# Optimization experiments

Measured on AMD Instinct MI355X. Metric: run time of the kernel, lower is better.

The kernel has to match this reference:

```python
import jax, jax.numpy as jnp
import numpy as np


def color_bin(x, n_bins):
    """Per-image 3D color histogram over n_bins**3 flat bins.
    x: [B, 3, H, W] float in ~[-1, 1]. Returns [B, n_bins**3] float32.
    """
    B, C, H, W = x.shape
    n_tot = n_bins ** 3
    # torch color_bins: i*(2/n_bins) - 1 for i in 1..n_bins-1
    boundaries = jnp.arange(1, n_bins, dtype=jnp.float32) * (2.0 / n_bins) - 1.0
    # torch.bucketize(right=False) == searchsorted side='left'
    idx = jnp.searchsorted(boundaries, x.reshape(B, C, H * W), side='left')  # [B,3,HW] int
    scale = jnp.array([1, n_bins, n_bins ** 2], dtype=idx.dtype)
    flat = jnp.einsum('bcp,c->bp', idx, scale)  # [B, HW], values in [0, n_tot)
    # torch.histc(bins, n_tot, min=0, max=n_tot-1) on exact integers == bincount
    hist = jax.vmap(lambda f: jnp.bincount(f, length=n_tot))(flat)
    return hist.astype(jnp.float32) / (H * W)


def setup_inputs() -> dict:
    key = jax.random.key(0)
    k1, k2 = jax.random.split(key)
    inp = jax.random.normal(k1, (8, 3, 1024, 1024), dtype=jnp.float32)
    style = jax.random.normal(k2, (1, 3, 1024, 1024), dtype=jnp.float32)
    return {"input": inp, "style_image": style, "n_bins": 16}


def reference(input, style_image, n_bins):
    # target histogram from the style image (detached in torch; ints anyway)
    target = color_bin(style_image, n_bins).squeeze(0)  # [n_tot]
    cols = color_bin(input, n_bins)                     # [B, n_tot]
    # F.l1_loss(cols, target.repeat(B, 1)) with mean reduction
    loss = jnp.mean(jnp.abs(cols - target[None, :]))
    return loss
```

## Files before the change

### kernel.cpp

```cpp
#include <hip/hip_runtime.h>

#define HW      (1024 * 1024)
#define HW4     (HW / 4)
#define NBINS   4096
#define NIMG    9
#define BPI     128
#define THREADS 256
#define F4_PER_BLOCK (HW4 / BPI)
#define NSTAGE  (F4_PER_BLOCK / (2 * THREADS))
#define RBLOCKS 256

typedef float f4 __attribute__((ext_vector_type(4)));

__device__ __forceinline__ int bin16(float x) {
    int lo = 0;
    if (0.0f < x) lo = 8;
    if ((float)(lo + 4) * 0.125f - 1.0f < x) lo += 4;
    if ((float)(lo + 2) * 0.125f - 1.0f < x) lo += 2;
    if ((float)(lo + 1) * 0.125f - 1.0f < x) lo += 1;
    return lo;
}

__device__ __forceinline__ int bin3(float r, float g, float b) {
    return bin16(r) + 16 * bin16(g) + 256 * bin16(b);
}

__device__ __forceinline__ void acc4(int* lh, f4 r, f4 g, f4 b) {
    atomicAdd(&lh[bin3(r.x, g.x, b.x)], 1);
    atomicAdd(&lh[bin3(r.y, g.y, b.y)], 1);
    atomicAdd(&lh[bin3(r.z, g.z, b.z)], 1);
    atomicAdd(&lh[bin3(r.w, g.w, b.w)], 1);
}

__global__ __launch_bounds__(THREADS, 4) void hist_kernel(
        const float* __restrict__ input,
        const float* __restrict__ style,
        unsigned short* __restrict__ part,
        unsigned long long* __restrict__ gsum) {
    __shared__ int lh[NBINS];
    const int img = blockIdx.y;
    const int blk = blockIdx.x;
    if (img == 8 && blk == 0 && threadIdx.x == 0) *gsum = 0ULL;
    const float* base = (img < 8) ? (input + (size_t)img * 3 * HW) : style;

    for (int i = threadIdx.x; i < NBINS; i += THREADS) lh[i] = 0;
    __syncthreads();

    const f4* c0 = (const f4*)(base);
    const f4* c1 = (const f4*)(base + HW);
    const f4* c2 = (const f4*)(base + 2 * HW);
    const int start = blk * F4_PER_BLOCK + threadIdx.x;

    f4 buf[2][6];
    auto load_stage = [&](int s, f4* d) {
        const int p0 = start + s * 2 * THREADS;
        const int p1 = p0 + THREADS;
        d[0] = c0[p0]; d[1] = c1[p0]; d[2] = c2[p0];
        d[3] = c0[p1]; d[4] = c1[p1]; d[5] = c2[p1];
    };

    load_stage(0, buf[0]);
#pragma unroll
    for (int s = 0; s < NSTAGE; ++s) {
        if (s + 1 < NSTAGE) load_stage(s + 1, buf[(s + 1) & 1]);
        f4* d = buf[s & 1];
        acc4(lh, d[0], d[1], d[2]);
        acc4(lh, d[3], d[4], d[5]);
    }
    __syncthreads();

    uint4* dst = (uint4*)(part + ((size_t)img * BPI + blk) * NBINS);
    for (int i = threadIdx.x; i < NBINS / 8; i += THREADS) {
        uint4 v;
        v.x = (unsigned)lh[8 * i]     | ((unsigned)lh[8 * i + 1] << 16);
        v.y = (unsigned)lh[8 * i + 2] | ((unsigned)lh[8 * i + 3] << 16);
        v.z = (unsigned)lh[8 * i + 4] | ((unsigned)lh[8 * i + 5] << 16);
        v.w = (unsigned)lh[8 * i + 6] | ((unsigned)lh[8 * i + 7] << 16);
        dst[i] = v;
    }
}

__global__ __launch_bounds__(THREADS) void reduce_loss_kernel(
        const unsigned short* __restrict__ part,
        unsigned long long* __restrict__ gsum,
        float* __restrict__ out) {
    __shared__ int tred[4][16];
    __shared__ int tgt[16];
    __shared__ int warr[4];
    const int lane = threadIdx.x & 63;
    const int w    = threadIdx.x >> 6;
    const int c    = lane & 1;
    const int p    = lane >> 1;
    const int b0   = blockIdx.x * 16;

    auto qptr = [&](int img, int pg) {
        return (const uint4*)(part + ((size_t)(img * BPI + pg) * NBINS)
                              + b0 + 8 * c);
    };

    {
        uint4 v = *qptr(8, p + 32 * w);
        int v8[8];
        v8[0] = v.x & 0xFFFF; v8[1] = v.x >> 16;
        v8[2] = v.y & 0xFFFF; v8[3] = v.y >> 16;
        v8[4] = v.z & 0xFFFF; v8[5] = v.z >> 16;
        v8[6] = v.w & 0xFFFF; v8[7] = v.w >> 16;
#pragma unroll
        for (int m = 2; m <= 32; m <<= 1) {
#pragma unroll
            for (int i = 0; i < 8; ++i) v8[i] += __shfl_xor(v8[i], m, 64);
        }
        if (lane < 2) {
#pragma unroll
            for (int i = 0; i < 8; ++i) tred[w][8 * c + i] = v8[i];
        }
    }
    __syncthreads();
    if (threadIdx.x < 16) {
        tgt[threadIdx.x] = tred[0][threadIdx.x] + tred[1][threadIdx.x]
                         + tred[2][threadIdx.x] + tred[3][threadIdx.x];
    }
    __syncthreads();

    int acc = 0;
#pragma unroll
    for (int ph = 0; ph < 2; ++ph) {
        const int img = w + 4 * ph;
        uint4 a  = *qptr(img, p);
        uint4 b  = *qptr(img, p + 32);
        uint4 cc = *qptr(img, p + 64);
        uint4 d  = *qptr(img, p + 96);
        uint4 s;
        s.x = a.x + b.x + cc.x + d.x;
        s.y = a.y + b.y + cc.y + d.y;
        s.z = a.z + b.z + cc.z + d.z;
        s.w = a.w + b.w + cc.w + d.w;
        int v8[8];
        v8[0] = s.x & 0xFFFF; v8[1] = s.x >> 16;
        v8[2] = s.y & 0xFFFF; v8[3] = s.y >> 16;
        v8[4] = s.z & 0xFFFF; v8[5] = s.z >> 16;
        v8[6] = s.w & 0xFFFF; v8[7] = s.w >> 16;
#pragma unroll
        for (int m = 2; m <= 32; m <<= 1) {
#pragma unroll
            for (int i = 0; i < 8; ++i) v8[i] += __shfl_xor(v8[i], m, 64);
        }
        if (lane < 2) {
#pragma unroll
            for (int i = 0; i < 8; ++i) {
                const int dd = v8[i] - tgt[8 * c + i];
                acc += (dd < 0) ? -dd : dd;
            }
        }
    }

    acc += __shfl_xor(acc, 1, 64);
    if (lane == 0) warr[w] = acc;
    __syncthreads();
    if (threadIdx.x == 0) {
        const unsigned long long bacc =
            (unsigned long long)(warr[0] + warr[1] + warr[2] + warr[3]);
        const unsigned long long old =
            atomicAdd(gsum, bacc + (1ULL << 40));
        if ((old >> 40) == RBLOCKS - 1) {
            const unsigned long long total =
                (old & ((1ULL << 40) - 1)) + bacc;
            out[0] = (float)((double)total / 34359738368.0);
        }
    }
}

extern "C" void kernel_launch(void* const* d_in, const int* in_sizes, int n_in,
                              void* d_out, int out_size, void* d_ws, size_t ws_size,
                              hipStream_t stream) {
    const float* input = (const float*)d_in[0];
    const float* style = (const float*)d_in[1];
    unsigned short* part = (unsigned short*)d_ws;
    unsigned long long* gsum = (unsigned long long*)((char*)d_ws +
                        (size_t)NIMG * BPI * NBINS * sizeof(unsigned short));

    hipLaunchKernelGGL(hist_kernel, dim3(BPI, NIMG), dim3(THREADS), 0, stream,
                       input, style, part, gsum);
    hipLaunchKernelGGL(reduce_loss_kernel, dim3(RBLOCKS), dim3(THREADS),
                       0, stream, part, gsum, (float*)d_out);
}
```

Before: 169.6 us.

## Use two privatized LDS histogram copies per block and halve blocks per image

```diff
diff --git a/kernel.cpp b/kernel.cpp
--- a/kernel.cpp
+++ b/kernel.cpp
@@ -4,10 +4,11 @@
 #define HW4     (HW / 4)
 #define NBINS   4096
 #define NIMG    9
-#define BPI     128
+#define BPI     64
 #define THREADS 256
 #define F4_PER_BLOCK (HW4 / BPI)
 #define NSTAGE  (F4_PER_BLOCK / (2 * THREADS))
+#define HSTRIDE 4104
 #define RBLOCKS 256
 
 typedef float f4 __attribute__((ext_vector_type(4)));
@@ -37,14 +38,16 @@
         const float* __restrict__ style,
         unsigned short* __restrict__ part,
         unsigned long long* __restrict__ gsum) {
-    __shared__ int lh[NBINS];
+    __shared__ int lh[2 * HSTRIDE];
     const int img = blockIdx.y;
     const int blk = blockIdx.x;
     if (img == 8 && blk == 0 && threadIdx.x == 0) *gsum = 0ULL;
     const float* base = (img < 8) ? (input + (size_t)img * 3 * HW) : style;
 
-    for (int i = threadIdx.x; i < NBINS; i += THREADS) lh[i] = 0;
+    for (int i = threadIdx.x; i < 2 * HSTRIDE; i += THREADS) lh[i] = 0;
     __syncthreads();
+
+    int* h = lh + (threadIdx.x & 1) * HSTRIDE;
 
     const f4* c0 = (const f4*)(base);
     const f4* c1 = (const f4*)(base + HW);
@@ -64,18 +67,26 @@
     for (int s = 0; s < NSTAGE; ++s) {
         if (s + 1 < NSTAGE) load_stage(s + 1, buf[(s + 1) & 1]);
         f4* d = buf[s & 1];
-        acc4(lh, d[0], d[1], d[2]);
-        acc4(lh, d[3], d[4], d[5]);
+        acc4(h, d[0], d[1], d[2]);
+        acc4(h, d[3], d[4], d[5]);
     }
     __syncthreads();
 
     uint4* dst = (uint4*)(part + ((size_t)img * BPI + blk) * NBINS);
     for (int i = threadIdx.x; i < NBINS / 8; i += THREADS) {
+        unsigned s0 = lh[8 * i]     + lh[HSTRIDE + 8 * i];
+        unsigned s1 = lh[8 * i + 1] + lh[HSTRIDE + 8 * i + 1];
+        unsigned s2 = lh[8 * i + 2] + lh[HSTRIDE + 8 * i + 2];
+        unsigned s3 = lh[8 * i + 3] + lh[HSTRIDE + 8 * i + 3];
+        unsigned s4 = lh[8 * i + 4] + lh[HSTRIDE + 8 * i + 4];
+        unsigned s5 = lh[8 * i + 5] + lh[HSTRIDE + 8 * i + 5];
+        unsigned s6 = lh[8 * i + 6] + lh[HSTRIDE + 8 * i + 6];
+        unsigned s7 = lh[8 * i + 7] + lh[HSTRIDE + 8 * i + 7];
         uint4 v;
-        v.x = (unsigned)lh[8 * i]     | ((unsigned)lh[8 * i + 1] << 16);
-        v.y = (unsigned)lh[8 * i + 2] | ((unsigned)lh[8 * i + 3] << 16);
-        v.z = (unsigned)lh[8 * i + 4] | ((unsigned)lh[8 * i + 5] << 16);
-        v.w = (unsigned)lh[8 * i + 6] | ((unsigned)lh[8 * i + 7] << 16);
+        v.x = s0 | (s1 << 16);
+        v.y = s2 | (s3 << 16);
+        v.z = s4 | (s5 << 16);
+        v.w = s6 | (s7 << 16);
         dst[i] = v;
     }
 }
@@ -84,7 +95,6 @@
         const unsigned short* __restrict__ part,
         unsigned long long* __restrict__ gsum,
         float* __restrict__ out) {
-    __shared__ int tred[4][16];
     __shared__ int tgt[16];
     __shared__ int warr[4];
     const int lane = threadIdx.x & 63;
@@ -97,14 +107,22 @@
         return (const uint4*)(part + ((size_t)(img * BPI + pg) * NBINS)
                               + b0 + 8 * c);
     };
+    auto unpack_add = [&](uint4 a, uint4 b, int* v8) {
+        v8[0] = (int)(a.x & 0xFFFF) + (int)(b.x & 0xFFFF);
+        v8[1] = (int)(a.x >> 16)    + (int)(b.x >> 16);
+        v8[2] = (int)(a.y & 0xFFFF) + (int)(b.y & 0xFFFF);
+        v8[3] = (int)(a.y >> 16)    + (int)(b.y >> 16);
+        v8[4] = (int)(a.z & 0xFFFF) + (int)(b.z & 0xFFFF);
+        v8[5] = (int)(a.z >> 16)    + (int)(b.z >> 16);
+        v8[6] = (int)(a.w & 0xFFFF) + (int)(b.w & 0xFFFF);
+        v8[7] = (int)(a.w >> 16)    + (int)(b.w >> 16);
+    };
 
     {
-        uint4 v = *qptr(8, p + 32 * w);
+        uint4 a = *qptr(8, p);
+        uint4 b = *qptr(8, p + 32);
         int v8[8];
-        v8[0] = v.x & 0xFFFF; v8[1] = v.x >> 16;
-        v8[2] = v.y & 0xFFFF; v8[3] = v.y >> 16;
-        v8[4] = v.z & 0xFFFF; v8[5] = v.z >> 16;
-        v8[6] = v.w & 0xFFFF; v8[7] = v.w >> 16;
+        unpack_add(a, b, v8);
 #pragma unroll
         for (int m = 2; m <= 32; m <<= 1) {
 #pragma unroll
@@ -112,13 +130,8 @@
         }
         if (lane < 2) {
 #pragma unroll
-            for (int i = 0; i < 8; ++i) tred[w][8 * c + i] = v8[i];
+            for (int i = 0; i < 8; ++i) tgt[8 * c + i] = v8[i];
         }
-    }
-    __syncthreads();
-    if (threadIdx.x < 16) {
-        tgt[threadIdx.x] = tred[0][threadIdx.x] + tred[1][threadIdx.x]
-                         + tred[2][threadIdx.x] + tred[3][threadIdx.x];
     }
     __syncthreads();
 
@@ -126,20 +139,10 @@
 #pragma unroll
     for (int ph = 0; ph < 2; ++ph) {
         const int img = w + 4 * ph;
-        uint4 a  = *qptr(img, p);
-        uint4 b  = *qptr(img, p + 32);
-        uint4 cc = *qptr(img, p + 64);
-        uint4 d  = *qptr(img, p + 96);
-        uint4 s;
-        s.x = a.x + b.x + cc.x + d.x;
-        s.y = a.y + b.y + cc.y + d.y;
-        s.z = a.z + b.z + cc.z + d.z;
-        s.w = a.w + b.w + cc.w + d.w;
+        uint4 a = *qptr(img, p);
+        uint4 b = *qptr(img, p + 32);
         int v8[8];
-        v8[0] = s.x & 0xFFFF; v8[1] = s.x >> 16;
-        v8[2] = s.y & 0xFFFF; v8[3] = s.y >> 16;
-        v8[4] = s.z & 0xFFFF; v8[5] = s.z >> 16;
-        v8[6] = s.w & 0xFFFF; v8[7] = s.w >> 16;
+        unpack_add(a, b, v8);
 #pragma unroll
         for (int m = 2; m <= 32; m <<= 1) {
 #pragma unroll
```

Result: no change. 172.2 us (+1.5%).
